# Performance work log

Measured on AMD Instinct MI355X. Metric: run time of the kernel, lower is better.

The kernel has to match this reference:

```python
import jax, jax.numpy as jnp
import numpy as np
from jax.scipy.special import logsumexp

ENTROPY_REG = 0.1   # entropy regularization (temperature)
N_ITERS = 100       # Sinkhorn-Knopp iterations (fixed, jit-friendly)


def setup_inputs() -> dict:
    key = jax.random.key(0)
    B, n = 128, 512
    X = jax.random.normal(key, (B, n, n), dtype=jnp.float32)
    return {"X": X}


def _sinkhorn_project(X):
    """Entropy-regularized projection of Q=X onto the doubly-stochastic
    polytope (Birkhoff polytope). This is the hand-written Sinkhorn-Knopp
    replacement for the generic CvxpyLayer conic solve: alternating row/col
    normalization of exp(X / entropy_reg), carried out in log-space for
    numerical stability. Output P satisfies P @ 1 = 1, 1^T P = 1^T, 0<=P<=1.
    """
    logP = X / ENTROPY_REG  # [B, n, n]

    def step(logP, _):
        # row normalization (each row sums to 1)
        logP = logP - logsumexp(logP, axis=-1, keepdims=True)
        # column normalization (each column sums to 1)
        logP = logP - logsumexp(logP, axis=-2, keepdims=True)
        return logP, None

    logP, _ = jax.lax.scan(step, logP, None, length=N_ITERS)
    return jnp.exp(logP)


def reference(X):
    return _sinkhorn_project(X)
```

## Files before the change

### kernel.cpp

```cpp
#include <hip/hip_runtime.h>
#include <math.h>

#define N 512
#define NITERS 100

__global__ __launch_bounds__(1024, 1)
void sinkhorn_fused(const float* __restrict__ X, float* __restrict__ P) {
    __shared__ float v_s[N];
    __shared__ float u_s[N];
    __shared__ float c_lds[16 * N];

    const int tid  = threadIdx.x;
    const int lane = tid & 63;
    const int wave = tid >> 6;

    const size_t base = (size_t)blockIdx.x * N * N;
    const float* __restrict__ A = X + base;
    float* __restrict__ out = P + base;

    if (tid < N) v_s[tid] = 0.0f;
    __syncthreads();

    const float SC = 10.0f;
    const size_t RSTEP = (size_t)16 * N;

    for (int it = 0; it < NITERS; ++it) {
        float4 vv0 = *(const float4*)(v_s + 4 * lane);
        float4 vv1 = *(const float4*)(v_s + 256 + 4 * lane);
        float c0 = 0.f, c1 = 0.f, c2 = 0.f, c3 = 0.f,
              c4 = 0.f, c5 = 0.f, c6 = 0.f, c7 = 0.f;
        const bool last = (it == NITERS - 1);

        const float* rp = A + (size_t)wave * N;
        float4 a0 = ((const float4*)rp)[lane];
        float4 a1 = ((const float4*)rp)[lane + 64];

        #pragma unroll 1
        for (int r = wave; r < N; r += 16) {
            float4 b0, b1;
            if (r + 16 < N) {
                const float4* np = (const float4*)(rp + RSTEP);
                b0 = np[lane];
                b1 = np[lane + 64];
            }
            float x0 = fmaf(a0.x, SC, -vv0.x);
            float x1 = fmaf(a0.y, SC, -vv0.y);
            float x2 = fmaf(a0.z, SC, -vv0.z);
            float x3 = fmaf(a0.w, SC, -vv0.w);
            float x4 = fmaf(a1.x, SC, -vv1.x);
            float x5 = fmaf(a1.y, SC, -vv1.y);
            float x6 = fmaf(a1.z, SC, -vv1.z);
            float x7 = fmaf(a1.w, SC, -vv1.w);
            float mx = fmaxf(fmaxf(fmaxf(x0, x1), fmaxf(x2, x3)),
                             fmaxf(fmaxf(x4, x5), fmaxf(x6, x7)));
            #pragma unroll
            for (int o = 32; o > 0; o >>= 1) mx = fmaxf(mx, __shfl_xor(mx, o, 64));
            float e0 = __expf(x0 - mx), e1 = __expf(x1 - mx);
            float e2 = __expf(x2 - mx), e3 = __expf(x3 - mx);
            float e4 = __expf(x4 - mx), e5 = __expf(x5 - mx);
            float e6 = __expf(x6 - mx), e7 = __expf(x7 - mx);
            float s = ((e0 + e1) + (e2 + e3)) + ((e4 + e5) + (e6 + e7));
            #pragma unroll
            for (int o = 32; o > 0; o >>= 1) s += __shfl_xor(s, o, 64);
            float invS = __builtin_amdgcn_rcpf(s);
            c0 = fmaf(e0, invS, c0); c1 = fmaf(e1, invS, c1);
            c2 = fmaf(e2, invS, c2); c3 = fmaf(e3, invS, c3);
            c4 = fmaf(e4, invS, c4); c5 = fmaf(e5, invS, c5);
            c6 = fmaf(e6, invS, c6); c7 = fmaf(e7, invS, c7);
            if (last && lane == 0) u_s[r] = mx + __logf(s);
            a0 = b0; a1 = b1;
            rp += RSTEP;
        }

        *(float4*)(c_lds + wave * N + 4 * lane)       = make_float4(c0, c1, c2, c3);
        *(float4*)(c_lds + wave * N + 256 + 4 * lane) = make_float4(c4, c5, c6, c7);
        __syncthreads();
        if (tid < N) {
            float cs = 0.f;
            #pragma unroll
            for (int w = 0; w < 16; ++w) cs += c_lds[w * N + tid];
            v_s[tid] += __logf(fmaxf(cs, 1e-30f));
        }
        __syncthreads();
    }

    {
        float4 vv0 = *(const float4*)(v_s + 4 * lane);
        float4 vv1 = *(const float4*)(v_s + 256 + 4 * lane);
        #pragma unroll 1
        for (int r = wave; r < N; r += 16) {
            const float ur = u_s[r];
            const float4* rowp = (const float4*)(A + (size_t)r * N);
            float4* outp = (float4*)(out + (size_t)r * N);
            float4 a0 = rowp[lane];
            float4 a1 = rowp[lane + 64];
            float4 o0, o1;
            o0.x = __expf(fmaf(a0.x, SC, -vv0.x) - ur);
            o0.y = __expf(fmaf(a0.y, SC, -vv0.y) - ur);
            o0.z = __expf(fmaf(a0.z, SC, -vv0.z) - ur);
            o0.w = __expf(fmaf(a0.w, SC, -vv0.w) - ur);
            o1.x = __expf(fmaf(a1.x, SC, -vv1.x) - ur);
            o1.y = __expf(fmaf(a1.y, SC, -vv1.y) - ur);
            o1.z = __expf(fmaf(a1.z, SC, -vv1.z) - ur);
            o1.w = __expf(fmaf(a1.w, SC, -vv1.w) - ur);
            outp[lane]      = o0;
            outp[lane + 64] = o1;
        }
    }
}

extern "C" void kernel_launch(void* const* d_in, const int* in_sizes, int n_in,
                              void* d_out, int out_size, void* d_ws, size_t ws_size,
                              hipStream_t stream) {
    const float* X = (const float*)d_in[0];
    float* P = (float*)d_out;
    const int batch = in_sizes[0] / (N * N);
    hipLaunchKernelGGL(sinkhorn_fused, dim3(batch), dim3(1024), 0, stream, X, P);
}
```

Baseline: 2.436 ms.

## Switch Sinkhorn to multiplicative scaling over a precomputed bf16 kernel matrix

```diff
diff --git a/kernel.cpp b/kernel.cpp
--- a/kernel.cpp
+++ b/kernel.cpp
@@ -3,11 +3,21 @@
 
 #define N 512
 #define NITERS 100
+#define SC 10.0f
+
+__device__ __forceinline__ unsigned int pack_bf16(float a, float b) {
+    unsigned int ua = __float_as_uint(a);
+    unsigned int ub = __float_as_uint(b);
+    ua = (ua + 0x7fffu + ((ua >> 16) & 1u)) >> 16;
+    ub = (ub + 0x7fffu + ((ub >> 16) & 1u)) >> 16;
+    return ua | (ub << 16);
+}
 
 __global__ __launch_bounds__(1024, 1)
-void sinkhorn_fused(const float* __restrict__ X, float* __restrict__ P) {
-    __shared__ float v_s[N];
-    __shared__ float u_s[N];
+void sinkhorn_mult(const float* __restrict__ X, float* __restrict__ P) {
+    __shared__ float w_s[N];
+    __shared__ float m_s[N];
+    __shared__ float lnS_s[N];
     __shared__ float c_lds[16 * N];
 
     const int tid  = threadIdx.x;
@@ -15,50 +25,60 @@
     const int wave = tid >> 6;
 
     const size_t base = (size_t)blockIdx.x * N * N;
-    const float* __restrict__ A = X + base;
-    float* __restrict__ out = P + base;
+    const float* __restrict__ A   = X + base;
+    float*       __restrict__ out = P + base;
+    unsigned short* __restrict__ Kb = (unsigned short*)(P + base);
 
-    if (tid < N) v_s[tid] = 0.0f;
+    if (tid < N) w_s[tid] = 1.0f;
+
+    #pragma unroll 1
+    for (int r = wave; r < N; r += 16) {
+        const float4* rowp = (const float4*)(A + (size_t)r * N);
+        float4 a0 = rowp[lane];
+        float4 a1 = rowp[lane + 64];
+        float x0 = a0.x * SC, x1 = a0.y * SC, x2 = a0.z * SC, x3 = a0.w * SC;
+        float x4 = a1.x * SC, x5 = a1.y * SC, x6 = a1.z * SC, x7 = a1.w * SC;
+        float mx = fmaxf(fmaxf(fmaxf(x0, x1), fmaxf(x2, x3)),
+                         fmaxf(fmaxf(x4, x5), fmaxf(x6, x7)));
+        #pragma unroll
+        for (int o = 32; o > 0; o >>= 1) mx = fmaxf(mx, __shfl_xor(mx, o, 64));
+        uint2 p0, p1;
+        p0.x = pack_bf16(__expf(x0 - mx), __expf(x1 - mx));
+        p0.y = pack_bf16(__expf(x2 - mx), __expf(x3 - mx));
+        p1.x = pack_bf16(__expf(x4 - mx), __expf(x5 - mx));
+        p1.y = pack_bf16(__expf(x6 - mx), __expf(x7 - mx));
+        uint2* krow = (uint2*)(Kb + (size_t)r * N);
+        krow[lane]      = p0;
+        krow[lane + 64] = p1;
+        if (lane == 0) m_s[r] = mx;
+    }
+    __threadfence();
     __syncthreads();
 
-    const float SC = 10.0f;
     const size_t RSTEP = (size_t)16 * N;
-
     for (int it = 0; it < NITERS; ++it) {
-        float4 vv0 = *(const float4*)(v_s + 4 * lane);
-        float4 vv1 = *(const float4*)(v_s + 256 + 4 * lane);
+        float4 w0 = *(const float4*)(w_s + 8 * lane);
+        float4 w1 = *(const float4*)(w_s + 8 * lane + 4);
         float c0 = 0.f, c1 = 0.f, c2 = 0.f, c3 = 0.f,
               c4 = 0.f, c5 = 0.f, c6 = 0.f, c7 = 0.f;
         const bool last = (it == NITERS - 1);
 
-        const float* rp = A + (size_t)wave * N;
-        float4 a0 = ((const float4*)rp)[lane];
-        float4 a1 = ((const float4*)rp)[lane + 64];
-
+        const unsigned short* kp = Kb + (size_t)wave * N;
+        uint4 kq = ((const uint4*)kp)[lane];
         #pragma unroll 1
         for (int r = wave; r < N; r += 16) {
-            float4 b0, b1;
-            if (r + 16 < N) {
-                const float4* np = (const float4*)(rp + RSTEP);
-                b0 = np[lane];
-                b1 = np[lane + 64];
-            }
-            float x0 = fmaf(a0.x, SC, -vv0.x);
-            float x1 = fmaf(a0.y, SC, -vv0.y);
-            float x2 = fmaf(a0.z, SC, -vv0.z);
-            float x3 = fmaf(a0.w, SC, -vv0.w);
-            float x4 = fmaf(a1.x, SC, -vv1.x);
-            float x5 = fmaf(a1.y, SC, -vv1.y);
-            float x6 = fmaf(a1.z, SC, -vv1.z);
-            float x7 = fmaf(a1.w, SC, -vv1.w);
-            float mx = fmaxf(fmaxf(fmaxf(x0, x1), fmaxf(x2, x3)),
-                             fmaxf(fmaxf(x4, x5), fmaxf(x6, x7)));
-            #pragma unroll
-            for (int o = 32; o > 0; o >>= 1) mx = fmaxf(mx, __shfl_xor(mx, o, 64));
-            float e0 = __expf(x0 - mx), e1 = __expf(x1 - mx);
-            float e2 = __expf(x2 - mx), e3 = __expf(x3 - mx);
-            float e4 = __expf(x4 - mx), e5 = __expf(x5 - mx);
-            float e6 = __expf(x6 - mx), e7 = __expf(x7 - mx);
+            uint4 nq;
+            if (r + 16 < N) nq = ((const uint4*)(kp + RSTEP))[lane];
+            float f0 = __uint_as_float(kq.x << 16);
+            float f1 = __uint_as_float(kq.x & 0xffff0000u);
+            float f2 = __uint_as_float(kq.y << 16);
+            float f3 = __uint_as_float(kq.y & 0xffff0000u);
+            float f4 = __uint_as_float(kq.z << 16);
+            float f5 = __uint_as_float(kq.z & 0xffff0000u);
+            float f6 = __uint_as_float(kq.w << 16);
+            float f7 = __uint_as_float(kq.w & 0xffff0000u);
+            float e0 = f0 * w0.x, e1 = f1 * w0.y, e2 = f2 * w0.z, e3 = f3 * w0.w;
+            float e4 = f4 * w1.x, e5 = f5 * w1.y, e6 = f6 * w1.z, e7 = f7 * w1.w;
             float s = ((e0 + e1) + (e2 + e3)) + ((e4 + e5) + (e6 + e7));
             #pragma unroll
             for (int o = 32; o > 0; o >>= 1) s += __shfl_xor(s, o, 64);
@@ -67,45 +87,50 @@
             c2 = fmaf(e2, invS, c2); c3 = fmaf(e3, invS, c3);
             c4 = fmaf(e4, invS, c4); c5 = fmaf(e5, invS, c5);
             c6 = fmaf(e6, invS, c6); c7 = fmaf(e7, invS, c7);
-            if (last && lane == 0) u_s[r] = mx + __logf(s);
-            a0 = b0; a1 = b1;
-            rp += RSTEP;
+            if (last && lane == 0) lnS_s[r] = __logf(s);
+            kq = nq; kp += RSTEP;
         }
 
-        *(float4*)(c_lds + wave * N + 4 * lane)       = make_float4(c0, c1, c2, c3);
-        *(float4*)(c_lds + wave * N + 256 + 4 * lane) = make_float4(c4, c5, c6, c7);
+        *(float4*)(c_lds + wave * N + 8 * lane)     = make_float4(c0, c1, c2, c3);
+        *(float4*)(c_lds + wave * N + 8 * lane + 4) = make_float4(c4, c5, c6, c7);
         __syncthreads();
         if (tid < N) {
             float cs = 0.f;
             #pragma unroll
             for (int w = 0; w < 16; ++w) cs += c_lds[w * N + tid];
-            v_s[tid] += __logf(fmaxf(cs, 1e-30f));
+            w_s[tid] = w_s[tid] / fmaxf(cs, 1e-38f);
         }
         __syncthreads();
     }
 
-    {
-        float4 vv0 = *(const float4*)(v_s + 4 * lane);
-        float4 vv1 = *(const float4*)(v_s + 256 + 4 * lane);
-        #pragma unroll 1
-        for (int r = wave; r < N; r += 16) {
-            const float ur = u_s[r];
-            const float4* rowp = (const float4*)(A + (size_t)r * N);
-            float4* outp = (float4*)(out + (size_t)r * N);
-            float4 a0 = rowp[lane];
-            float4 a1 = rowp[lane + 64];
-            float4 o0, o1;
-            o0.x = __expf(fmaf(a0.x, SC, -vv0.x) - ur);
-            o0.y = __expf(fmaf(a0.y, SC, -vv0.y) - ur);
-            o0.z = __expf(fmaf(a0.z, SC, -vv0.z) - ur);
-            o0.w = __expf(fmaf(a0.w, SC, -vv0.w) - ur);
-            o1.x = __expf(fmaf(a1.x, SC, -vv1.x) - ur);
-            o1.y = __expf(fmaf(a1.y, SC, -vv1.y) - ur);
-            o1.z = __expf(fmaf(a1.z, SC, -vv1.z) - ur);
-            o1.w = __expf(fmaf(a1.w, SC, -vv1.w) - ur);
-            outp[lane]      = o0;
-            outp[lane + 64] = o1;
-        }
+    float* g_s  = c_lds;
+    float* rt_s = c_lds + N;
+    if (tid < N) {
+        g_s[tid]  = __logf(w_s[tid]);
+        rt_s[tid] = -(m_s[tid] + lnS_s[tid]);
+    }
+    __syncthreads();
+
+    #pragma unroll 1
+    for (int r = wave; r < N; r += 16) {
+        const float rt = rt_s[r];
+        const float4* rowp = (const float4*)(A + (size_t)r * N);
+        float4 a0 = rowp[lane];
+        float4 a1 = rowp[lane + 64];
+        float4 g0 = *(const float4*)(g_s + 4 * lane);
+        float4 g1 = *(const float4*)(g_s + 256 + 4 * lane);
+        float4 o0, o1;
+        o0.x = __expf(fmaf(a0.x, SC, rt) + g0.x);
+        o0.y = __expf(fmaf(a0.y, SC, rt) + g0.y);
+        o0.z = __expf(fmaf(a0.z, SC, rt) + g0.z);
+        o0.w = __expf(fmaf(a0.w, SC, rt) + g0.w);
+        o1.x = __expf(fmaf(a1.x, SC, rt) + g1.x);
+        o1.y = __expf(fmaf(a1.y, SC, rt) + g1.y);
+        o1.z = __expf(fmaf(a1.z, SC, rt) + g1.z);
+        o1.w = __expf(fmaf(a1.w, SC, rt) + g1.w);
+        float4* outp = (float4*)(out + (size_t)r * N);
+        outp[lane]      = o0;
+        outp[lane + 64] = o1;
     }
 }
 
@@ -115,5 +140,5 @@
     const float* X = (const float*)d_in[0];
     float* P = (float*)d_out;
     const int batch = in_sizes[0] / (N * N);
-    hipLaunchKernelGGL(sinkhorn_fused, dim3(batch), dim3(1024), 0, stream, X, P);
+    hipLaunchKernelGGL(sinkhorn_mult, dim3(batch), dim3(1024), 0, stream, X, P);
 }
```

Measured after the change: 2.183 ms. 1.12x faster.
